# Kernel tuning notes

Hardware: AMD Instinct MI355X
Metric: run time of the kernel (lower is better)

Reference implementation:

```python
import jax, jax.numpy as jnp
import numpy as np

B, T, D = 8, 2048, 512
S = 4                 # n_slots
SLOT_DIM = D          # cfg.slot_dim defaults to d_model
SE = 8                # state_embed_dim
GH = 64               # gate_hidden
EMA = 0.99
SIGMA_FLOOR = 1e-3
OPEN2CLOSING, CLOSING2LOCKED, UNLOCK = 0.1, 0.03, 0.25
GAINS = jnp.array([1.0, 0.5, 0.1], dtype=jnp.float32)  # OPEN, CLOSING, LOCKED


def _glorot(k, shape, fi, fo):
    b = (6.0 / (fi + fo)) ** 0.5
    return jax.random.uniform(k, shape, jnp.float32, -b, b)


def setup_inputs() -> dict:
    key = jax.random.key(0)
    ks = jax.random.split(key, 8)
    gate_in = D + 1 + SE  # [h, z, state_embed]
    return {
        'h_seq': jax.random.normal(ks[0], (B, T, D), jnp.float32),
        'pred_W': _glorot(ks[1], (S, D, D), D, D),
        'pred_b': jnp.zeros((S, D), jnp.float32),
        'gate_W1': _glorot(ks[2], (S, gate_in, GH), gate_in, GH),
        'gate_b1': jnp.zeros((S, GH), jnp.float32),
        'gate_W2': _glorot(ks[3], (S, GH, 1), GH, 1),
        'gate_b2': jnp.zeros((S, 1), jnp.float32),
        'write_W': _glorot(ks[4], (S, D, SLOT_DIM), D, SLOT_DIM),
        'write_b': jnp.zeros((S, SLOT_DIM), jnp.float32),
        'w0': jnp.zeros((S, SLOT_DIM), jnp.float32),
        'state_embed': jax.random.normal(ks[5], (3, SE), jnp.float32),
    }


def reference(h_seq, pred_W, pred_b, gate_W1, gate_b1, gate_W2, gate_b2,
              write_W, write_b, w0, state_embed):
    Bb, Tt, Dd = h_seq.shape
    h_det = jax.lax.stop_gradient(h_seq)
    # per-slot next-step predictions (input detached, as in torch): (B,T,S,D)
    preds = jnp.einsum('btd,sdo->btso', h_det, pred_W) + pred_b
    # prediction emitted at t-1 targets h_t
    pred_prev = jnp.concatenate([jnp.zeros_like(preds[:, :1]), preds[:, :-1]], axis=1)
    valid = jnp.arange(Tt) > 0  # no surprise signal at t=0

    m0 = jnp.broadcast_to(w0, (Bb, S, SLOT_DIM)).astype(h_seq.dtype)
    carry0 = (m0,
              jnp.zeros((S,), jnp.float32),       # mu
              jnp.ones((S,), jnp.float32),        # sigma
              jnp.full((S,), 0.5, jnp.float32),   # gate_ema
              jnp.zeros((S,), jnp.int32))         # slot_state

    def step(carry, xs):
        m, mu, sigma, gate_ema, state = carry
        h_t, p_prev, ok = xs  # (B,D), (B,S,D), scalar bool
        # prediction-error surprise per slot
        err = jnp.sqrt(jnp.sum((p_prev - h_t[:, None, :]) ** 2, axis=-1) + 1e-8)  # (B,S)
        err = jnp.where(ok, err, 0.0)
        z = (err - mu) / jnp.maximum(sigma, SIGMA_FLOOR)  # (B,S)
        # gate MLP over [h, z, state_embed]
        se = state_embed[state]  # (S,SE)
        gin = jnp.concatenate([
            jnp.broadcast_to(h_t[:, None, :], (Bb, S, Dd)),
            z[..., None],
            jnp.broadcast_to(se[None], (Bb, S, SE))], axis=-1)
        hid = jax.nn.relu(jnp.einsum('bsi,sih->bsh', gin, gate_W1) + gate_b1)
        g = jax.nn.sigmoid(jnp.einsum('bsh,sho->bso', hid, gate_W2) + gate_b2)[..., 0]  # (B,S)
        # state-dependent write gain (OPEN/CLOSING/LOCKED)
        g_eff = g * GAINS[state]
        w_enc = jnp.einsum('bd,sdo->bso', h_t, write_W) + write_b
        m = (1.0 - g_eff[..., None]) * m + g_eff[..., None] * w_enc
        read = m.reshape(Bb, S * SLOT_DIM)
        # homeostatic bookkeeping (buffers: non-differentiable, EMA)
        err_s = jax.lax.stop_gradient(err)
        mu_n = jnp.where(ok, EMA * mu + (1 - EMA) * err_s.mean(0), mu)
        sigma_n = jnp.where(ok, EMA * sigma + (1 - EMA) * jnp.abs(err_s - mu).mean(0), sigma)
        gate_ema_n = EMA * gate_ema + (1 - EMA) * jax.lax.stop_gradient(g).mean(0)
        # state machine transitions on gate EMA
        st = jnp.where((state == 0) & (gate_ema_n < OPEN2CLOSING), 1, state)
        st = jnp.where((state == 1) & (gate_ema_n < CLOSING2LOCKED), 2,
             jnp.where((state == 1) & (gate_ema_n > UNLOCK), 0, st))
        st = jnp.where((state == 2) & (gate_ema_n > UNLOCK), 0, st)
        return (m, mu_n, sigma_n, gate_ema_n, st), read

    xs = (jnp.swapaxes(h_seq, 0, 1), jnp.swapaxes(pred_prev, 0, 1), valid)
    _, reads = jax.lax.scan(step, carry0, xs)
    return jnp.swapaxes(reads, 0, 1)  # (B,T,S*SLOT_DIM)
```

## Files before the change

kernel.cpp:

```cpp
#include <hip/hip_runtime.h>
#include <hip/hip_bf16.h>

#define Bb 8
#define Tt 2048
#define Dd 512
#define Ss 4
#define GHh 64
#define NCHUNK 32

typedef __hip_bfloat16 bf16;
typedef short bf16x8 __attribute__((ext_vector_type(8)));
typedef float f32x4 __attribute__((ext_vector_type(4)));
__device__ __forceinline__ float b2f(bf16 x){ return __bfloat162float(x); }

#define GLOAD_LDS16(g, l) \
  __builtin_amdgcn_global_load_lds((const __attribute__((address_space(1))) unsigned int*)(const void*)(g), \
                                   (__attribute__((address_space(3))) unsigned int*)(l), 16, 0, 0)

__global__ __launch_bounds__(256) void k0a_cvt(const float* __restrict__ h, bf16* __restrict__ hb){
  int i = (blockIdx.x*256 + threadIdx.x)*4;
  float4 v = *reinterpret_cast<const float4*>(&h[i]);
  hb[i+0] = __float2bfloat16(v.x);
  hb[i+1] = __float2bfloat16(v.y);
  hb[i+2] = __float2bfloat16(v.z);
  hb[i+3] = __float2bfloat16(v.w);
}

__global__ __launch_bounds__(256) void k0b_pack(const float* __restrict__ predW,
    const float* __restrict__ writeW, const float* __restrict__ gateW1, bf16* __restrict__ Wt){
  __shared__ float tile[32][33];
  int k0 = blockIdx.x*32, n0 = blockIdx.y*32;
  int tx = threadIdx.x & 31, ty = threadIdx.x >> 5;
  #pragma unroll
  for (int p = 0; p < 4; ++p) {
    int kk = ty + p*8;
    int n = n0 + tx, k = k0 + kk;
    float v;
    if (n < 2048)      { int s=n>>9, o=n&511;              v = predW[((size_t)s*512+k)*512+o]; }
    else if (n < 4096) { int n2=n-2048; int s=n2>>9,o=n2&511; v = writeW[((size_t)s*512+k)*512+o]; }
    else               { int n2=n-4096; int s=n2>>6,hh=n2&63; v = gateW1[((size_t)s*521+k)*64+hh]; }
    tile[kk][tx] = v;
  }
  __syncthreads();
  #pragma unroll
  for (int p = 0; p < 4; ++p) {
    int nn = ty + p*8;
    Wt[(size_t)(n0+nn)*512 + k0 + tx] = __float2bfloat16(tile[tx][nn]);
  }
}

__global__ __launch_bounds__(256) void k1_mfma(
    const bf16* __restrict__ hb, const bf16* __restrict__ Wt,
    const float* __restrict__ h, const float* __restrict__ predb, const float* __restrict__ writeb,
    bf16* __restrict__ wenc, float* __restrict__ hg, float* __restrict__ errsq)
{
  __shared__ bf16 As[128*32];
  __shared__ bf16 Bs[128*32];
  const int tid = threadIdx.x;
  const int w = tid >> 6, lane = tid & 63;
  const int n0 = blockIdx.x * 128;
  const int row0 = blockIdx.y * 128;
  const int wm = w & 1, wn = w >> 1;
  const int mrow = lane & 15, kq = lane >> 4;

  f32x4 acc[4][4];
  #pragma unroll
  for (int i=0;i<4;++i)
    #pragma unroll
    for (int j=0;j<4;++j) acc[i][j] = (f32x4){0.f,0.f,0.f,0.f};

  const bf16* ga = hb + (size_t)(row0 + w*32 + (lane>>2))*512 + (lane&3)*8;
  const bf16* gb = Wt + (size_t)(n0  + w*32 + (lane>>2))*512 + (lane&3)*8;
  bf16* lA = &As[(w*32)*32];
  bf16* lB = &Bs[(w*32)*32];

  for (int k0 = 0; k0 < 512; k0 += 32) {
    GLOAD_LDS16(ga,           lA);
    GLOAD_LDS16(ga + 16*512,  lA + 16*32);
    GLOAD_LDS16(gb,           lB);
    GLOAD_LDS16(gb + 16*512,  lB + 16*32);
    ga += 32; gb += 32;
    __syncthreads();
    bf16x8 af[4], bfr[4];
    #pragma unroll
    for (int mi=0;mi<4;++mi)
      af[mi] = *reinterpret_cast<const bf16x8*>(&As[(wm*64 + mi*16 + mrow)*32 + kq*8]);
    #pragma unroll
    for (int ni=0;ni<4;++ni)
      bfr[ni] = *reinterpret_cast<const bf16x8*>(&Bs[(wn*64 + ni*16 + mrow)*32 + kq*8]);
    #pragma unroll
    for (int mi=0;mi<4;++mi)
      #pragma unroll
      for (int ni=0;ni<4;++ni)
        acc[mi][ni] = __builtin_amdgcn_mfma_f32_16x16x32_bf16(af[mi], bfr[ni], acc[mi][ni], 0, 0, 0);
    __syncthreads();
  }

  if (n0 < 2048) {
    const int s = n0 >> 9;
    #pragma unroll
    for (int mi=0;mi<4;++mi) {
      #pragma unroll
      for (int reg=0;reg<4;++reg) {
        int r = row0 + wm*64 + mi*16 + kq*4 + reg;
        float sum = 0.f;
        if ((r & 2047) != 2047) {
          #pragma unroll
          for (int ni=0;ni<4;++ni) {
            int o = (n0 & 511) + wn*64 + ni*16 + mrow;
            float P = acc[mi][ni][reg] + predb[s*512 + o];
            float d = P - h[(size_t)(r+1)*512 + o];
            sum = fmaf(d, d, sum);
          }
        }
        #pragma unroll
        for (int off=1; off<16; off<<=1) sum += __shfl_xor(sum, off);
        if (mrow == 0 && (r & 2047) != 2047)
          atomicAdd(&errsq[(size_t)(r+1)*4 + s], sum);
      }
    }
  } else if (n0 < 4096) {
    #pragma unroll
    for (int mi=0;mi<4;++mi)
      #pragma unroll
      for (int ni=0;ni<4;++ni) {
        int n2 = n0 - 2048 + wn*64 + ni*16 + mrow;
        int s = n2 >> 9, o = n2 & 511;
        float wb = writeb[s*512 + o];
        #pragma unroll
        for (int reg=0;reg<4;++reg) {
          int r = row0 + wm*64 + mi*16 + kq*4 + reg;
          wenc[((size_t)r*4 + s)*512 + o] = __float2bfloat16(acc[mi][ni][reg] + wb);
        }
      }
  } else {
    #pragma unroll
    for (int mi=0;mi<4;++mi)
      #pragma unroll
      for (int ni=0;ni<4;++ni) {
        int n2 = n0 - 4096 + wn*64 + ni*16 + mrow;
        int s = n2 >> 6, hh = n2 & 63;
        #pragma unroll
        for (int reg=0;reg<4;++reg) {
          int r = row0 + wm*64 + mi*16 + kq*4 + reg;
          hg[((size_t)r*4 + s)*64 + hh] = acc[mi][ni][reg];
        }
      }
  }
}

__global__ void k2a_err(const float* __restrict__ errsq, float* __restrict__ err){
  int i = blockIdx.x*256 + threadIdx.x;
  int t = (i >> 2) & 2047;
  err[i] = (t > 0) ? sqrtf(errsq[i] + 1e-8f) : 0.f;
}

__global__ void k2b_em(const float* __restrict__ err, float* __restrict__ em){
  int i = blockIdx.x*256 + threadIdx.x;
  float sum = 0.f;
  #pragma unroll
  for (int b=0;b<8;++b) sum += err[b*8192 + i];
  em[i] = sum * 0.125f;
}

__global__ void k2c_scan(const float* __restrict__ in, float* __restrict__ outv, float init){
  __shared__ float s_in[8192];
  for (int i = threadIdx.x; i < 8192; i += 256) s_in[i] = in[i];
  __syncthreads();
  if (threadIdx.x < 4) {
    int s = threadIdx.x;
    float v = init;
    for (int t = 0; t < 2048; ++t) {
      outv[t*4+s] = v;
      if (t >= 1) v = 0.99f*v + 0.01f*s_in[t*4+s];
    }
  }
}

__global__ void k2d_sd(const float* __restrict__ err, const float* __restrict__ MU, float* __restrict__ sd){
  int i = blockIdx.x*256 + threadIdx.x;
  float mu = MU[i];
  float sum = 0.f;
  #pragma unroll
  for (int b=0;b<8;++b) sum += fabsf(err[b*8192 + i] - mu);
  sd[i] = sum * 0.125f;
}

__global__ void k2e_base(const float* __restrict__ gateW1, const float* __restrict__ semb,
                         const float* __restrict__ gateb1, float* __restrict__ base1){
  int i = blockIdx.x*256 + threadIdx.x;
  if (i < 768) {
    int hh = i & 63, k = (i >> 6) % 3, s = i / 192;
    float acc = gateb1[s*64 + hh];
    #pragma unroll
    for (int e = 0; e < 8; ++e)
      acc = fmaf(semb[k*8+e], gateW1[((size_t)s*521 + 513 + e)*64 + hh], acc);
    base1[i] = acc;
  }
}

__global__ void k3_gall(const float* __restrict__ hg, const float* __restrict__ err,
    const float* __restrict__ MU, const float* __restrict__ SIG,
    const float* __restrict__ gateW1, const float* __restrict__ base1,
    const float* __restrict__ gateW2, const float* __restrict__ gateb2,
    float* __restrict__ g_all)
{
  int i = blockIdx.x*256 + threadIdx.x;
  int k = i % 3;
  int bts = i / 3;
  int s = bts & 3;
  int t = (bts >> 2) & 2047;
  float e = err[bts];
  float z = (e - MU[t*4+s]) / fmaxf(SIG[t*4+s], 1e-3f);
  const float* hgp = &hg[(size_t)bts*64];
  const float* b1p = &base1[(s*3 + k)*64];
  const float* w1zp = &gateW1[((size_t)s*521 + 512)*64];
  const float* w2p = &gateW2[s*64];
  float logit = 0.f;
  for (int hh = 0; hh < 64; ++hh) {
    float hid = hgp[hh] + z*w1zp[hh] + b1p[hh];
    hid = fmaxf(hid, 0.f);
    logit = fmaf(hid, w2p[hh], logit);
  }
  logit += gateb2[s];
  g_all[i] = 1.f/(1.f + expf(-logit));
}

__global__ void k3b_gm(const float* __restrict__ g_all, float* __restrict__ gm){
  int i = blockIdx.x*256 + threadIdx.x;
  float sum = 0.f;
  #pragma unroll
  for (int b=0;b<8;++b) sum += g_all[((size_t)b*8192 + i/3)*3 + (i%3)];
  gm[i] = sum * 0.125f;
}

__global__ void k4_scan(const float* __restrict__ gm, int* __restrict__ states){
  __shared__ float s_gm[6144];
  float ema = 0.5f; int st = 0;
  for (int c = 0; c < 4; ++c) {
    __syncthreads();
    for (int i = threadIdx.x; i < 6144; i += 256) s_gm[i] = gm[c*6144 + i];
    __syncthreads();
    if (threadIdx.x < 4) {
      int s = threadIdx.x;
      for (int tt = 0; tt < 512; ++tt) {
        int t = c*512 + tt;
        states[t*4+s] = st;
        float g = s_gm[tt*12 + s*3 + st];
        ema = 0.99f*ema + 0.01f*g;
        int ns = st;
        if (st == 0 && ema < 0.1f) ns = 1;
        if (st == 1) ns = (ema < 0.03f) ? 2 : ((ema > 0.25f) ? 0 : 1);
        if (st == 2 && ema > 0.25f) ns = 0;
        st = ns;
      }
    }
  }
}

__global__ void k5_a(const float* __restrict__ g_all, const int* __restrict__ states, float* __restrict__ a){
  int i = blockIdx.x*256 + threadIdx.x;
  int ts = i & 8191;
  int st = states[ts];
  float gain = (st == 0) ? 1.f : ((st == 1) ? 0.5f : 0.1f);
  a[i] = g_all[(size_t)i*3 + st] * gain;
}

__global__ __launch_bounds__(512) void k6_pass1(const float* __restrict__ a, const bf16* __restrict__ wenc,
      float* __restrict__ q, float* __restrict__ Pc){
  int c = blockIdx.x, s = blockIdx.y, b = blockIdx.z;
  int d = threadIdx.x;
  __shared__ float s_a[64];
  if (d < 64) s_a[d] = a[(size_t)(b*2048 + c*64 + d)*4 + s];
  __syncthreads();
  float qv = 0.f, p = 1.f;
  #pragma unroll 4
  for (int i = 0; i < 64; ++i) {
    float av = s_a[i];
    float w = b2f(wenc[((size_t)(b*2048 + c*64 + i)*4 + s)*512 + d]);
    qv = (1.f - av)*qv + av*w;
    p *= (1.f - av);
  }
  q[((size_t)(b*4+s)*32 + c)*512 + d] = qv;
  if (d == 0) Pc[(b*4+s)*32 + c] = p;
}

__global__ __launch_bounds__(512) void k7_bound(const float* __restrict__ q, const float* __restrict__ Pc,
      const float* __restrict__ w0, float* __restrict__ m_start){
  int s = blockIdx.x, b = blockIdx.y, d = threadIdx.x;
  float m = w0[s*512 + d];
  for (int c = 0; c < 32; ++c) {
    m_start[((size_t)(b*4+s)*32 + c)*512 + d] = m;
    m = Pc[(b*4+s)*32 + c]*m + q[((size_t)(b*4+s)*32 + c)*512 + d];
  }
}

__global__ __launch_bounds__(512) void k8_pass2(const float* __restrict__ a, const bf16* __restrict__ wenc,
      const float* __restrict__ m_start, float* __restrict__ out){
  int c = blockIdx.x, s = blockIdx.y, b = blockIdx.z;
  int d = threadIdx.x;
  __shared__ float s_a[64];
  if (d < 64) s_a[d] = a[(size_t)(b*2048 + c*64 + d)*4 + s];
  __syncthreads();
  float m = m_start[((size_t)(b*4+s)*32 + c)*512 + d];
  #pragma unroll 4
  for (int i = 0; i < 64; ++i) {
    int t = c*64 + i;
    float av = s_a[i];
    float w = b2f(wenc[((size_t)(b*2048 + t)*4 + s)*512 + d]);
    m = (1.f - av)*m + av*w;
    out[((size_t)b*2048 + t)*2048 + s*512 + d] = m;
  }
}

extern "C" void kernel_launch(void* const* d_in, const int* in_sizes, int n_in,
                              void* d_out, int out_size, void* d_ws, size_t ws_size,
                              hipStream_t stream) {
  (void)in_sizes; (void)n_in; (void)out_size; (void)ws_size;
  const float* h      = (const float*)d_in[0];
  const float* predW  = (const float*)d_in[1];
  const float* predb  = (const float*)d_in[2];
  const float* gateW1 = (const float*)d_in[3];
  const float* gateb1 = (const float*)d_in[4];
  const float* gateW2 = (const float*)d_in[5];
  const float* gateb2 = (const float*)d_in[6];
  const float* writeW = (const float*)d_in[7];
  const float* writeb = (const float*)d_in[8];
  const float* w0     = (const float*)d_in[9];
  const float* semb   = (const float*)d_in[10];
  float* out = (float*)d_out;

  char* ws = (char*)d_ws;
  size_t off = 0;
  auto alloc = [&](size_t bytes) -> char* {
    char* p = ws + off; off += (bytes + 255) / 256 * 256; return p;
  };
  bf16*  wenc   = (bf16*) alloc((size_t)Bb*Tt*Ss*Dd*2);
  float* hg     = (float*)alloc((size_t)Bb*Tt*Ss*GHh*4);
  bf16*  hb     = (bf16*) alloc((size_t)Bb*Tt*Dd*2);
  bf16*  Wt     = (bf16*) alloc((size_t)4352*512*2);
  float* errsq  = (float*)alloc((size_t)Bb*Tt*Ss*4);
  float* err    = (float*)alloc((size_t)Bb*Tt*Ss*4);
  float* em     = (float*)alloc((size_t)Tt*Ss*4);
  float* MU     = (float*)alloc((size_t)Tt*Ss*4);
  float* sd     = (float*)alloc((size_t)Tt*Ss*4);
  float* SIG    = (float*)alloc((size_t)Tt*Ss*4);
  float* base1  = (float*)alloc((size_t)Ss*3*GHh*4);
  float* g_all  = (float*)alloc((size_t)Bb*Tt*Ss*3*4);
  float* gm     = (float*)alloc((size_t)Tt*Ss*3*4);
  int*   states = (int*)  alloc((size_t)Tt*Ss*4);
  float* av     = (float*)alloc((size_t)Bb*Tt*Ss*4);
  float* Pc     = (float*)alloc((size_t)Bb*Ss*NCHUNK*4);
  float* q      = (float*)alloc((size_t)Bb*Ss*NCHUNK*Dd*4);
  float* mst    = (float*)alloc((size_t)Bb*Ss*NCHUNK*Dd*4);

  hipMemsetAsync(errsq, 0, (size_t)Bb*Tt*Ss*4, stream);

  k0a_cvt<<<(Bb*Tt*Dd)/(256*4), 256, 0, stream>>>(h, hb);
  dim3 g0b(16, 136);
  k0b_pack<<<g0b, 256, 0, stream>>>(predW, writeW, gateW1, Wt);
  dim3 g1(34, 128);
  k1_mfma<<<g1, 256, 0, stream>>>(hb, Wt, h, predb, writeb, wenc, hg, errsq);
  k2a_err<<<(Bb*Tt*Ss)/256, 256, 0, stream>>>(errsq, err);
  k2b_em<<<(Tt*Ss)/256, 256, 0, stream>>>(err, em);
  k2c_scan<<<1, 256, 0, stream>>>(em, MU, 0.f);
  k2d_sd<<<(Tt*Ss)/256, 256, 0, stream>>>(err, MU, sd);
  k2c_scan<<<1, 256, 0, stream>>>(sd, SIG, 1.f);
  k2e_base<<<3, 256, 0, stream>>>(gateW1, semb, gateb1, base1);
  k3_gall<<<(Bb*Tt*Ss*3)/256, 256, 0, stream>>>(hg, err, MU, SIG, gateW1, base1, gateW2, gateb2, g_all);
  k3b_gm<<<(Tt*Ss*3)/256, 256, 0, stream>>>(g_all, gm);
  k4_scan<<<1, 256, 0, stream>>>(gm, states);
  k5_a<<<(Bb*Tt*Ss)/256, 256, 0, stream>>>(g_all, states, av);
  dim3 g6(NCHUNK, Ss, Bb);
  k6_pass1<<<g6, 512, 0, stream>>>(av, wenc, q, Pc);
  dim3 g7(Ss, Bb);
  k7_bound<<<g7, 512, 0, stream>>>(q, Pc, w0, mst);
  k8_pass2<<<g6, 512, 0, stream>>>(av, wenc, mst, out);
}
```

Baseline: 663.9 us.

## Double-buffer swizzled GEMM tiles and vectorize chunked memory-scan passes

```diff
diff --git a/kernel.cpp b/kernel.cpp
--- a/kernel.cpp
+++ b/kernel.cpp
@@ -6,7 +6,8 @@
 #define Dd 512
 #define Ss 4
 #define GHh 64
-#define NCHUNK 32
+#define NCHUNK 64
+#define CH 32
 
 typedef __hip_bfloat16 bf16;
 typedef short bf16x8 __attribute__((ext_vector_type(8)));
@@ -54,8 +55,8 @@
     const float* __restrict__ h, const float* __restrict__ predb, const float* __restrict__ writeb,
     bf16* __restrict__ wenc, float* __restrict__ hg, float* __restrict__ errsq)
 {
-  __shared__ bf16 As[128*32];
-  __shared__ bf16 Bs[128*32];
+  __shared__ bf16 As[2][128*64];
+  __shared__ bf16 Bs[2][128*64];
   const int tid = threadIdx.x;
   const int w = tid >> 6, lane = tid & 63;
   const int n0 = blockIdx.x * 128;
@@ -69,30 +70,51 @@
     #pragma unroll
     for (int j=0;j<4;++j) acc[i][j] = (f32x4){0.f,0.f,0.f,0.f};
 
-  const bf16* ga = hb + (size_t)(row0 + w*32 + (lane>>2))*512 + (lane&3)*8;
-  const bf16* gb = Wt + (size_t)(n0  + w*32 + (lane>>2))*512 + (lane&3)*8;
-  bf16* lA = &As[(w*32)*32];
-  bf16* lB = &Bs[(w*32)*32];
-
-  for (int k0 = 0; k0 < 512; k0 += 32) {
-    GLOAD_LDS16(ga,           lA);
-    GLOAD_LDS16(ga + 16*512,  lA + 16*32);
-    GLOAD_LDS16(gb,           lB);
-    GLOAD_LDS16(gb + 16*512,  lB + 16*32);
-    ga += 32; gb += 32;
-    __syncthreads();
-    bf16x8 af[4], bfr[4];
-    #pragma unroll
-    for (int mi=0;mi<4;++mi)
-      af[mi] = *reinterpret_cast<const bf16x8*>(&As[(wm*64 + mi*16 + mrow)*32 + kq*8]);
-    #pragma unroll
-    for (int ni=0;ni<4;++ni)
-      bfr[ni] = *reinterpret_cast<const bf16x8*>(&Bs[(wn*64 + ni*16 + mrow)*32 + kq*8]);
-    #pragma unroll
-    for (int mi=0;mi<4;++mi)
-      #pragma unroll
-      for (int ni=0;ni<4;++ni)
-        acc[mi][ni] = __builtin_amdgcn_mfma_f32_16x16x32_bf16(af[mi], bfr[ni], acc[mi][ni], 0, 0, 0);
+  const int srow  = lane >> 3;
+  const int sslot = (lane & 7) ^ srow;
+  const bf16* gaBase = hb + (size_t)(row0 + w*32 + srow)*512 + sslot*8;
+  const bf16* gbBase = Wt + (size_t)(n0  + w*32 + srow)*512 + sslot*8;
+
+  auto STAGE = [&](int buf, int kstep){
+    const bf16* ga = gaBase + kstep*64;
+    const bf16* gb = gbBase + kstep*64;
+    bf16* lA = &As[buf][(w*32)*64];
+    bf16* lB = &Bs[buf][(w*32)*64];
+    #pragma unroll
+    for (int i=0;i<4;++i) {
+      GLOAD_LDS16(ga + (size_t)i*8*512, lA + i*8*64);
+      GLOAD_LDS16(gb + (size_t)i*8*512, lB + i*8*64);
+    }
+  };
+
+  auto COMPUTE = [&](int buf){
+    #pragma unroll
+    for (int kk=0; kk<2; ++kk) {
+      bf16x8 af[4], bfr[4];
+      #pragma unroll
+      for (int mi=0;mi<4;++mi) {
+        int r = wm*64 + mi*16 + mrow;
+        af[mi] = *reinterpret_cast<const bf16x8*>(&As[buf][r*64 + (((kk*4+kq) ^ (r&7))<<3)]);
+      }
+      #pragma unroll
+      for (int ni=0;ni<4;++ni) {
+        int r = wn*64 + ni*16 + mrow;
+        bfr[ni] = *reinterpret_cast<const bf16x8*>(&Bs[buf][r*64 + (((kk*4+kq) ^ (r&7))<<3)]);
+      }
+      #pragma unroll
+      for (int mi=0;mi<4;++mi)
+        #pragma unroll
+        for (int ni=0;ni<4;++ni)
+          acc[mi][ni] = __builtin_amdgcn_mfma_f32_16x16x32_bf16(af[mi], bfr[ni], acc[mi][ni], 0, 0, 0);
+    }
+  };
+
+  STAGE(0, 0);
+  __syncthreads();
+  #pragma unroll
+  for (int t = 0; t < 8; ++t) {
+    if (t < 7) STAGE((t+1)&1, t+1);
+    COMPUTE(t&1);
     __syncthreads();
   }
 
@@ -266,50 +288,65 @@
   a[i] = g_all[(size_t)i*3 + st] * gain;
 }
 
-__global__ __launch_bounds__(512) void k6_pass1(const float* __restrict__ a, const bf16* __restrict__ wenc,
+__global__ __launch_bounds__(64) void k6_pass1(const float* __restrict__ a, const bf16* __restrict__ wenc,
       float* __restrict__ q, float* __restrict__ Pc){
   int c = blockIdx.x, s = blockIdx.y, b = blockIdx.z;
-  int d = threadIdx.x;
-  __shared__ float s_a[64];
-  if (d < 64) s_a[d] = a[(size_t)(b*2048 + c*64 + d)*4 + s];
+  int d0 = threadIdx.x << 3;
+  __shared__ float s_a[CH];
+  if (threadIdx.x < CH) s_a[threadIdx.x] = a[(size_t)(b*2048 + c*CH + threadIdx.x)*4 + s];
   __syncthreads();
-  float qv = 0.f, p = 1.f;
+  float qv[8];
+  #pragma unroll
+  for (int j=0;j<8;++j) qv[j] = 0.f;
+  float p = 1.f;
+  const bf16* wp = &wenc[((size_t)(b*2048 + c*CH)*4 + s)*512 + d0];
   #pragma unroll 4
-  for (int i = 0; i < 64; ++i) {
+  for (int i = 0; i < CH; ++i) {
     float av = s_a[i];
-    float w = b2f(wenc[((size_t)(b*2048 + c*64 + i)*4 + s)*512 + d]);
-    qv = (1.f - av)*qv + av*w;
-    p *= (1.f - av);
-  }
-  q[((size_t)(b*4+s)*32 + c)*512 + d] = qv;
-  if (d == 0) Pc[(b*4+s)*32 + c] = p;
+    bf16x8 wv = *reinterpret_cast<const bf16x8*>(wp + (size_t)i*4*512);
+    float om = 1.f - av;
+    #pragma unroll
+    for (int j=0;j<8;++j) qv[j] = fmaf(om, qv[j], av*b2f(((const bf16*)&wv)[j]));
+    p *= om;
+  }
+  float* qp = &q[((size_t)(b*4+s)*NCHUNK + c)*512 + d0];
+  #pragma unroll
+  for (int j=0;j<8;++j) qp[j] = qv[j];
+  if (threadIdx.x == 0) Pc[(b*4+s)*NCHUNK + c] = p;
 }
 
 __global__ __launch_bounds__(512) void k7_bound(const float* __restrict__ q, const float* __restrict__ Pc,
       const float* __restrict__ w0, float* __restrict__ m_start){
   int s = blockIdx.x, b = blockIdx.y, d = threadIdx.x;
   float m = w0[s*512 + d];
-  for (int c = 0; c < 32; ++c) {
-    m_start[((size_t)(b*4+s)*32 + c)*512 + d] = m;
-    m = Pc[(b*4+s)*32 + c]*m + q[((size_t)(b*4+s)*32 + c)*512 + d];
-  }
-}
-
-__global__ __launch_bounds__(512) void k8_pass2(const float* __restrict__ a, const bf16* __restrict__ wenc,
+  for (int c = 0; c < NCHUNK; ++c) {
+    m_start[((size_t)(b*4+s)*NCHUNK + c)*512 + d] = m;
+    m = Pc[(b*4+s)*NCHUNK + c]*m + q[((size_t)(b*4+s)*NCHUNK + c)*512 + d];
+  }
+}
+
+__global__ __launch_bounds__(64) void k8_pass2(const float* __restrict__ a, const bf16* __restrict__ wenc,
       const float* __restrict__ m_start, float* __restrict__ out){
   int c = blockIdx.x, s = blockIdx.y, b = blockIdx.z;
-  int d = threadIdx.x;
-  __shared__ float s_a[64];
-  if (d < 64) s_a[d] = a[(size_t)(b*2048 + c*64 + d)*4 + s];
+  int d0 = threadIdx.x << 3;
+  __shared__ float s_a[CH];
+  if (threadIdx.x < CH) s_a[threadIdx.x] = a[(size_t)(b*2048 + c*CH + threadIdx.x)*4 + s];
   __syncthreads();
-  float m = m_start[((size_t)(b*4+s)*32 + c)*512 + d];
-  #pragma unroll 4
-  for (int i = 0; i < 64; ++i) {
-    int t = c*64 + i;
+  float m[8];
+  const float* msp = &m_start[((size_t)(b*4+s)*NCHUNK + c)*512 + d0];
+  #pragma unroll
+  for (int j=0;j<8;++j) m[j] = msp[j];
+  const bf16* wp = &wenc[((size_t)(b*2048 + c*CH)*4 + s)*512 + d0];
+  float* op = &out[((size_t)(b*2048 + c*CH))*2048 + s*512 + d0];
+  #pragma unroll 2
+  for (int i = 0; i < CH; ++i) {
     float av = s_a[i];
-    float w = b2f(wenc[((size_t)(b*2048 + t)*4 + s)*512 + d]);
-    m = (1.f - av)*m + av*w;
-    out[((size_t)b*2048 + t)*2048 + s*512 + d] = m;
+    bf16x8 wv = *reinterpret_cast<const bf16x8*>(wp + (size_t)i*4*512);
+    float om = 1.f - av;
+    #pragma unroll
+    for (int j=0;j<8;++j) m[j] = fmaf(om, m[j], av*b2f(((const bf16*)&wv)[j]));
+    #pragma unroll
+    for (int j=0;j<8;++j) op[(size_t)i*2048 + j] = m[j];
   }
 }
 
@@ -372,8 +409,8 @@
   k4_scan<<<1, 256, 0, stream>>>(gm, states);
   k5_a<<<(Bb*Tt*Ss)/256, 256, 0, stream>>>(g_all, states, av);
   dim3 g6(NCHUNK, Ss, Bb);
-  k6_pass1<<<g6, 512, 0, stream>>>(av, wenc, q, Pc);
+  k6_pass1<<<g6, 64, 0, stream>>>(av, wenc, q, Pc);
   dim3 g7(Ss, Bb);
   k7_bound<<<g7, 512, 0, stream>>>(q, Pc, w0, mst);
-  k8_pass2<<<g6, 512, 0, stream>>>(av, wenc, mst, out);
-}
+  k8_pass2<<<g6, 64, 0, stream>>>(av, wenc, mst, out);
+}
```

New measurement: 646.5 us. -2.6%, faster.
